# Performance work log

Hardware: AMD Instinct MI355X
Metric: run time of the kernel (lower is better)

## Reference

```python
import jax, jax.numpy as jnp
import numpy as np

EMBED = 1024
HEADS = 16
HEAD_DIM = EMBED // HEADS


def setup_inputs() -> dict:
    key = jax.random.key(0)
    ks = jax.random.split(key, 12)
    B, S = 2, 2048
    inp = {
        "query": jax.random.normal(ks[0], (B, S, EMBED), dtype=jnp.float32),
        "key": jax.random.normal(ks[1], (B, S, EMBED), dtype=jnp.float32),
        "value": jax.random.normal(ks[2], (B, S, EMBED), dtype=jnp.float32),
        "mask": jnp.ones((B, 1, 1, S), dtype=jnp.int32),
    }
    scale = 1.0 / np.sqrt(EMBED)
    inp["Wq"] = jax.random.normal(ks[3], (EMBED, EMBED), dtype=jnp.float32) * scale
    inp["bq"] = jax.random.normal(ks[4], (EMBED,), dtype=jnp.float32) * 0.01
    inp["Wk"] = jax.random.normal(ks[5], (EMBED, EMBED), dtype=jnp.float32) * scale
    inp["bk"] = jax.random.normal(ks[6], (EMBED,), dtype=jnp.float32) * 0.01
    inp["Wv"] = jax.random.normal(ks[7], (EMBED, EMBED), dtype=jnp.float32) * scale
    inp["bv"] = jax.random.normal(ks[8], (EMBED,), dtype=jnp.float32) * 0.01
    inp["Wo"] = jax.random.normal(ks[9], (EMBED, EMBED), dtype=jnp.float32) * scale
    inp["bo"] = jax.random.normal(ks[10], (EMBED,), dtype=jnp.float32) * 0.01
    return inp


def reference(query, key, value, mask, Wq, bq, Wk, bk, Wv, bv, Wo, bo):
    N, Lq, _ = query.shape
    Lk = key.shape[1]
    # Linear projections (torch Linear: x @ W.T + b)
    q = (query @ Wq.T + bq).reshape(N, Lq, HEADS, HEAD_DIM)
    k = (key @ Wk.T + bk).reshape(N, Lk, HEADS, HEAD_DIM)
    v = (value @ Wv.T + bv).reshape(N, Lk, HEADS, HEAD_DIM)
    # scores: [N, H, Lq, Lk]
    energy = jnp.einsum("nqhd,nkhd->nhqk", q, k)
    energy = jnp.where(mask == 0, jnp.float32(-1e20), energy)
    # NOTE: original scales by sqrt(embedSize), not sqrt(head_dim)
    attn = jax.nn.softmax(energy / jnp.sqrt(jnp.float32(EMBED)), axis=3)
    out = jnp.einsum("nhqv,nvhd->nqhd", attn, v).reshape(N, Lq, EMBED)
    return out @ Wo.T + bo
```

## Files before the change

### kernel.cpp

```cpp
#include <hip/hip_runtime.h>
#include <stdint.h>

typedef unsigned short u16;
typedef __attribute__((ext_vector_type(8))) short short8;
typedef __attribute__((ext_vector_type(4))) short short4v;
typedef __attribute__((ext_vector_type(4))) float floatx4;

#define AS_GLOBAL __attribute__((address_space(1)))
#define AS_LDS    __attribute__((address_space(3)))

#define QSCALE 0.045084220f

__device__ __forceinline__ float bf2f(u16 u) {
  union { unsigned int i; float f; } x; x.i = ((unsigned int)u) << 16; return x.f;
}
__device__ __forceinline__ u16 f2bf(float f) {
  union { float f; unsigned int i; } x; x.f = f;
  unsigned int u = x.i;
  u += 0x7fffu + ((u >> 16) & 1u);
  return (u16)(u >> 16);
}
__device__ __forceinline__ u16 f2bf_fast(float f) {
  union { float f; unsigned int i; } x; x.f = f;
  return (u16)((x.i + 0x8000u) >> 16);
}

__device__ __forceinline__ int probe_is_f32(const void* p) {
  const unsigned int* w = (const unsigned int*)p;
  int cnt = 0;
#pragma unroll
  for (int i = 0; i < 64; ++i) {
    unsigned int lo = w[i] & 0xFFFFu;
    int e = (int)((lo >> 7) & 0xFFu);
    cnt += (e >= 117 && e <= 137) ? 1 : 0;
  }
  return cnt < 32;
}

__device__ __forceinline__ short8 ld8(const void* P, size_t off, int isf32) {
  if (isf32) {
    const float* q = (const float*)P + off;
    float4 x = *(const float4*)q;
    float4 y = *(const float4*)(q + 4);
    short8 r;
    r[0] = (short)f2bf(x.x); r[1] = (short)f2bf(x.y);
    r[2] = (short)f2bf(x.z); r[3] = (short)f2bf(x.w);
    r[4] = (short)f2bf(y.x); r[5] = (short)f2bf(y.y);
    r[6] = (short)f2bf(y.z); r[7] = (short)f2bf(y.w);
    return r;
  }
  return *(const short8*)((const u16*)P + off);
}

__device__ __forceinline__ float ldscalar(const void* P, size_t idx, int isf32) {
  return isf32 ? ((const float*)P)[idx] : bf2f(((const u16*)P)[idx]);
}

__global__ __launch_bounds__(256) void cvt7(
    const void* s0, const void* s1, const void* s2, const void* s3,
    const void* s4, const void* s5, const void* s6,
    u16* d0, u16* d1, u16* d2, u16* d3, u16* d4, u16* d5, u16* d6)
{
  const int z = blockIdx.y;
  const void* src; u16* dst; int n;
  switch (z) {
    case 0: src = s0; dst = d0; n = 4194304; break;
    case 1: src = s1; dst = d1; n = 4194304; break;
    case 2: src = s2; dst = d2; n = 4194304; break;
    case 3: src = s3; dst = d3; n = 1048576; break;
    case 4: src = s4; dst = d4; n = 1048576; break;
    case 5: src = s5; dst = d5; n = 1048576; break;
    default: src = s6; dst = d6; n = 1048576; break;
  }
  const int isf32 = probe_is_f32(src);
  for (int i = blockIdx.x * 256 + threadIdx.x; i * 4 < n; i += gridDim.x * 256) {
    if (isf32) {
      float4 x = ((const float4*)src)[i];
      short4v r;
      r[0] = (short)f2bf(x.x); r[1] = (short)f2bf(x.y);
      r[2] = (short)f2bf(x.z); r[3] = (short)f2bf(x.w);
      *(short4v*)(dst + (size_t)i * 4) = r;
    } else {
      *(short4v*)(dst + (size_t)i * 4) = ((const short4v*)src)[i];
    }
  }
}

__device__ __forceinline__ void gemm_core_bf16(
    const u16* __restrict__ A, const u16* __restrict__ W,
    u16* As, u16* Bs, floatx4 acc[4][4], int m0, int n0, int K, int tid)
{
  const int lane = tid & 63, wv = tid >> 6;
  const int wm = wv >> 1, wn = wv & 1;
  const int g = lane >> 4, ml = lane & 15;

  for (int kt = 0; kt < K; kt += 64) {
#pragma unroll
    for (int t = 0; t < 4; ++t) {
      int s = tid + t * 256;
      int row = s >> 3, chp = s & 7;
      int ch = chp ^ (row & 7);
      __builtin_amdgcn_global_load_lds(
          (const AS_GLOBAL unsigned int*)(A + (size_t)(m0 + row) * K + kt + ch * 8),
          (AS_LDS unsigned int*)(As + (size_t)((tid & 448) + t * 256) * 8), 16, 0, 0);
      __builtin_amdgcn_global_load_lds(
          (const AS_GLOBAL unsigned int*)(W + (size_t)(n0 + row) * K + kt + ch * 8),
          (AS_LDS unsigned int*)(Bs + (size_t)((tid & 448) + t * 256) * 8), 16, 0, 0);
    }
    __syncthreads();
#pragma unroll
    for (int kk = 0; kk < 2; ++kk) {
      short8 af[4], bf[4];
#pragma unroll
      for (int i = 0; i < 4; ++i) {
        int row = wm * 64 + i * 16 + ml;
        af[i] = *(const short8*)(As + row * 64 + (((kk << 2) + g) ^ (ml & 7)) * 8);
      }
#pragma unroll
      for (int j = 0; j < 4; ++j) {
        int row = wn * 64 + j * 16 + ml;
        bf[j] = *(const short8*)(Bs + row * 64 + (((kk << 2) + g) ^ (ml & 7)) * 8);
      }
#pragma unroll
      for (int i = 0; i < 4; ++i)
#pragma unroll
        for (int j = 0; j < 4; ++j)
          acc[i][j] = __builtin_amdgcn_mfma_f32_16x16x32_bf16(af[i], bf[j], acc[i][j], 0, 0, 0);
    }
    __syncthreads();
  }
}

__device__ __forceinline__ void gemm_core_cvt(
    const void* __restrict__ A, const void* __restrict__ W, int aF32, int bF32,
    u16* As, u16* Bs, floatx4 acc[4][4], int m0, int n0, int K, int tid)
{
  const int lane = tid & 63, wv = tid >> 6;
  const int wm = wv >> 1, wn = wv & 1;
  const int g = lane >> 4, ml = lane & 15;
  const int r0 = tid >> 2, kc = (tid & 3) << 3;
  const size_t offA0 = (size_t)(m0 + r0) * K + kc;
  const size_t offA1 = (size_t)(m0 + r0 + 64) * K + kc;
  const size_t offB0 = (size_t)(n0 + r0) * K + kc;
  const size_t offB1 = (size_t)(n0 + r0 + 64) * K + kc;
  u16* Al0 = As + tid * 8;  u16* Al1 = As + (tid + 256) * 8;
  u16* Bl0 = Bs + tid * 8;  u16* Bl1 = Bs + (tid + 256) * 8;
  for (int kt = 0; kt < K; kt += 32) {
    short8 a0 = ld8(A, offA0 + kt, aF32);
    short8 a1 = ld8(A, offA1 + kt, aF32);
    short8 b0 = ld8(W, offB0 + kt, bF32);
    short8 b1 = ld8(W, offB1 + kt, bF32);
    *(short8*)Al0 = a0;  *(short8*)Al1 = a1;
    *(short8*)Bl0 = b0;  *(short8*)Bl1 = b1;
    __syncthreads();
    short8 af[4], bf[4];
#pragma unroll
    for (int i = 0; i < 4; ++i)
      af[i] = *(const short8*)(As + (wm * 64 + i * 16 + ml) * 32 + g * 8);
#pragma unroll
    for (int j = 0; j < 4; ++j)
      bf[j] = *(const short8*)(Bs + (wn * 64 + j * 16 + ml) * 32 + g * 8);
#pragma unroll
    for (int i = 0; i < 4; ++i)
#pragma unroll
      for (int j = 0; j < 4; ++j)
        acc[i][j] = __builtin_amdgcn_mfma_f32_16x16x32_bf16(af[i], bf[j], acc[i][j], 0, 0, 0);
    __syncthreads();
  }
}

__device__ __forceinline__ void qkv_epilogue(
    floatx4 acc[4][4], const void* Bi, int cF32, u16* O, int m0, int n0,
    int tid, int z)
{
  const int lane = tid & 63, wv = tid >> 6;
  const int wm = wv >> 1, wn = wv & 1, g = lane >> 4, ml = lane & 15;
  const float sc = (z == 0) ? QSCALE : 1.0f;
#pragma unroll
  for (int j = 0; j < 4; ++j) {
    int gn = n0 + wn * 64 + j * 16 + ml;
    float bvv = ldscalar(Bi, (size_t)gn, cF32);
    int h = gn >> 6, d = gn & 63;
    if (z == 2) {
#pragma unroll
      for (int i = 0; i < 4; ++i) {
        int gm0 = m0 + wm * 64 + i * 16 + g * 4;
        int b = gm0 >> 11, s0 = gm0 & 2047;
        short4v pk;
#pragma unroll
        for (int r = 0; r < 4; ++r) pk[r] = (short)f2bf_fast(acc[i][j][r] + bvv);
        *(short4v*)(O + ((((size_t)b * 16 + h) * 64 + d) * 2048 + s0)) = pk;
      }
    } else {
#pragma unroll
      for (int i = 0; i < 4; ++i)
#pragma unroll
        for (int r = 0; r < 4; ++r) {
          int gm = m0 + wm * 64 + i * 16 + g * 4 + r;
          int b = gm >> 11, s = gm & 2047;
          O[(((size_t)b * 16 + h) * 2048 + s) * 64 + d] =
              f2bf_fast((acc[i][j][r] + bvv) * sc);
        }
    }
  }
}

__global__ __launch_bounds__(256) void qkv_gemm_bf16(
    const u16* __restrict__ Xq, const u16* __restrict__ Xk, const u16* __restrict__ Xv,
    const u16* __restrict__ Wq, const u16* __restrict__ Wk, const u16* __restrict__ Wv,
    const void* __restrict__ Bq, const void* __restrict__ Bk, const void* __restrict__ Bv,
    u16* __restrict__ Oq, u16* __restrict__ Ok, u16* __restrict__ Ov)
{
  __align__(16) __shared__ u16 As[8192];
  __align__(16) __shared__ u16 Bs[8192];
  const int z = blockIdx.z;
  const u16* X = (z == 0) ? Xq : (z == 1) ? Xk : Xv;
  const u16* W = (z == 0) ? Wq : (z == 1) ? Wk : Wv;
  const void* Bi = (z == 0) ? Bq : (z == 1) ? Bk : Bv;
  u16* O = (z == 0) ? Oq : (z == 1) ? Ok : Ov;
  const int cF32 = probe_is_f32(Bi);
  const int tid = threadIdx.x;
  const int m0 = blockIdx.y * 128, n0 = blockIdx.x * 128;
  floatx4 acc[4][4] = {};
  gemm_core_bf16(X, W, As, Bs, acc, m0, n0, 1024, tid);
  qkv_epilogue(acc, Bi, cF32, O, m0, n0, tid, z);
}

__global__ __launch_bounds__(256) void qkv_gemm_cvt(
    const void* __restrict__ Xq, const void* __restrict__ Xk, const void* __restrict__ Xv,
    const void* __restrict__ Wq, const void* __restrict__ Wk, const void* __restrict__ Wv,
    const void* __restrict__ Bq, const void* __restrict__ Bk, const void* __restrict__ Bv,
    u16* __restrict__ Oq, u16* __restrict__ Ok, u16* __restrict__ Ov)
{
  __align__(16) __shared__ u16 As[4096];
  __align__(16) __shared__ u16 Bs[4096];
  const int z = blockIdx.z;
  const void* X  = (z == 0) ? Xq : (z == 1) ? Xk : Xv;
  const void* W  = (z == 0) ? Wq : (z == 1) ? Wk : Wv;
  const void* Bi = (z == 0) ? Bq : (z == 1) ? Bk : Bv;
  u16* O = (z == 0) ? Oq : (z == 1) ? Ok : Ov;
  const int aF32 = probe_is_f32(X);
  const int bF32 = probe_is_f32(W);
  const int cF32 = probe_is_f32(Bi);
  const int tid = threadIdx.x;
  const int m0 = blockIdx.y * 128, n0 = blockIdx.x * 128;
  floatx4 acc[4][4] = {};
  gemm_core_cvt(X, W, aF32, bF32, As, Bs, acc, m0, n0, 1024, tid);
  qkv_epilogue(acc, Bi, cF32, O, m0, n0, tid, z);
}

__device__ __forceinline__ void out_epilogue(
    floatx4 acc[4][4], const void* Bi, int cF32, float* O, int m0, int n0, int tid)
{
  const int lane = tid & 63, wv = tid >> 6;
  const int wm = wv >> 1, wn = wv & 1, g = lane >> 4, ml = lane & 15;
#pragma unroll
  for (int j = 0; j < 4; ++j) {
    int gn = n0 + wn * 64 + j * 16 + ml;
    float bvv = ldscalar(Bi, (size_t)gn, cF32);
#pragma unroll
    for (int i = 0; i < 4; ++i)
#pragma unroll
      for (int r = 0; r < 4; ++r) {
        int gm = m0 + wm * 64 + i * 16 + g * 4 + r;
        O[(size_t)gm * 1024 + gn] = acc[i][j][r] + bvv;
      }
  }
}

__global__ __launch_bounds__(256) void out_gemm_bf16(
    const u16* __restrict__ X, const u16* __restrict__ W,
    const void* __restrict__ Bi, float* __restrict__ O)
{
  __align__(16) __shared__ u16 As[8192];
  __align__(16) __shared__ u16 Bs[8192];
  const int cF32 = probe_is_f32(Bi);
  const int tid = threadIdx.x;
  const int m0 = blockIdx.y * 128, n0 = blockIdx.x * 128;
  floatx4 acc[4][4] = {};
  gemm_core_bf16(X, W, As, Bs, acc, m0, n0, 1024, tid);
  out_epilogue(acc, Bi, cF32, O, m0, n0, tid);
}

__global__ __launch_bounds__(256) void out_gemm_cvt(
    const u16* __restrict__ X, const void* __restrict__ W,
    const void* __restrict__ Bi, float* __restrict__ O)
{
  __align__(16) __shared__ u16 As[4096];
  __align__(16) __shared__ u16 Bs[4096];
  const int bF32 = probe_is_f32(W);
  const int cF32 = probe_is_f32(Bi);
  const int tid = threadIdx.x;
  const int m0 = blockIdx.y * 128, n0 = blockIdx.x * 128;
  floatx4 acc[4][4] = {};
  gemm_core_cvt(X, W, 0, bF32, As, Bs, acc, m0, n0, 1024, tid);
  out_epilogue(acc, Bi, cF32, O, m0, n0, tid);
}

__global__ __launch_bounds__(256) void flash_attn(
    const u16* __restrict__ Q, const u16* __restrict__ K, const u16* __restrict__ V,
    const int* __restrict__ Mask, u16* __restrict__ O)
{
  __align__(16) __shared__ u16 Ks[128 * 64];
  __align__(16) __shared__ u16 Vt[64 * 128];
  __align__(16) __shared__ u16 Ps[4][16 * 136];
  __align__(16) __shared__ int Ms[128];
  __shared__ int Wok[4];

  const int qt = blockIdx.x;
  const int bh = blockIdx.y;
  const int b = bh >> 4, h = bh & 15;
  const int tid = threadIdx.x;
  const int lane = tid & 63, wv = tid >> 6;
  const int g = lane >> 4, ml = lane & 15;

  const size_t baseQ  = (((size_t)b * 16 + h) * 2048 + (size_t)qt * 64) * 64;
  const size_t baseKV = ((size_t)b * 16 + h) * 2048 * 64;

  {
    int la = 1;
#pragma unroll
    for (int i = 0; i < 8; ++i) la &= Mask[b * 2048 + tid * 8 + i];
    int wall = __all(la != 0);
    if (lane == 0) Wok[wv] = wall;
  }

  short8 qf[2];
#pragma unroll
  for (int ks = 0; ks < 2; ++ks)
    qf[ks] = *(const short8*)(Q + baseQ + (size_t)(wv * 16 + ml) * 64 + ks * 32 + g * 8);

  const u16* kg[4]; const u16* vg[4];
  u16* kl[4]; u16* vl[4];
#pragma unroll
  for (int t = 0; t < 4; ++t) {
    int s = tid + t * 256;
    int krow = s >> 3, kch = (s & 7) ^ (krow & 7);
    kg[t] = K + baseKV + (size_t)krow * 64 + kch * 8;
    int vd = s >> 4, vch = (s & 15) ^ (vd & 15);
    vg[t] = V + baseKV + (size_t)vd * 2048 + vch * 8;
    kl[t] = Ks + (size_t)((tid & 448) + t * 256) * 8;
    vl[t] = Vt + (size_t)((tid & 448) + t * 256) * 8;
  }

  __syncthreads();
  const bool maskall = Wok[0] && Wok[1] && Wok[2] && Wok[3];

  floatx4 oacc[4] = {};
  float lp[4] = {0.f, 0.f, 0.f, 0.f};

  for (int kv0 = 0; kv0 < 2048; kv0 += 128) {
    __syncthreads();
#pragma unroll
    for (int t = 0; t < 4; ++t) {
      __builtin_amdgcn_global_load_lds((const AS_GLOBAL unsigned int*)kg[t],
                                       (AS_LDS unsigned int*)kl[t], 16, 0, 0);
      __builtin_amdgcn_global_load_lds((const AS_GLOBAL unsigned int*)vg[t],
                                       (AS_LDS unsigned int*)vl[t], 16, 0, 0);
      kg[t] += 128 * 64;
      vg[t] += 128;
    }
    if (!maskall && tid < 128) Ms[tid] = Mask[b * 2048 + kv0 + tid];
    __syncthreads();

    float sv[8][4];
#pragma unroll
    for (int j = 0; j < 8; ++j) {
      floatx4 a = {0.f, 0.f, 0.f, 0.f};
      int row = j * 16 + ml;
#pragma unroll
      for (int ks = 0; ks < 2; ++ks) {
        short8 kb = *(const short8*)(Ks + row * 64 + ((((ks << 2) + g) ^ (ml & 7)) << 3));
        a = __builtin_amdgcn_mfma_f32_16x16x32_bf16(qf[ks], kb, a, 0, 0, 0);
      }
#pragma unroll
      for (int r = 0; r < 4; ++r) sv[j][r] = a[r];
    }
    if (!maskall) {
      int mok[8];
#pragma unroll
      for (int j = 0; j < 8; ++j) mok[j] = Ms[j * 16 + ml];
#pragma unroll
      for (int j = 0; j < 8; ++j)
#pragma unroll
        for (int r = 0; r < 4; ++r)
          sv[j][r] = (mok[j] == 0) ? -1.0e30f : sv[j][r];
    }

#pragma unroll
    for (int j = 0; j < 8; ++j)
#pragma unroll
      for (int r = 0; r < 4; ++r) {
        float p = __builtin_amdgcn_exp2f(fminf(sv[j][r], 80.f));
        sv[j][r] = p;
        lp[r] += p;
      }

#pragma unroll
    for (int j = 0; j < 8; ++j)
#pragma unroll
      for (int r = 0; r < 4; ++r)
        Ps[wv][(g * 4 + r) * 136 + j * 16 + ml] = f2bf_fast(sv[j][r]);

    __asm__ __volatile__("s_waitcnt lgkmcnt(0)" ::: "memory");

    short8 pa[4];
#pragma unroll
    for (int j2 = 0; j2 < 4; ++j2)
      pa[j2] = *(const short8*)(&Ps[wv][ml * 136 + j2 * 32 + g * 8]);
#pragma unroll
    for (int t = 0; t < 4; ++t)
#pragma unroll
      for (int j2 = 0; j2 < 4; ++j2) {
        short8 vb = *(const short8*)(Vt + (t * 16 + ml) * 128 + ((((j2 << 2) + g) ^ ml) << 3));
        oacc[t] = __builtin_amdgcn_mfma_f32_16x16x32_bf16(pa[j2], vb, oacc[t], 0, 0, 0);
      }
  }

  float inv[4];
#pragma unroll
  for (int r = 0; r < 4; ++r) {
    float l = lp[r];
    l += __shfl_xor(l, 1);
    l += __shfl_xor(l, 2);
    l += __shfl_xor(l, 4);
    l += __shfl_xor(l, 8);
    inv[r] = (l > 0.f) ? 1.0f / l : 0.f;
  }
#pragma unroll
  for (int t = 0; t < 4; ++t)
#pragma unroll
    for (int r = 0; r < 4; ++r) {
      int q = qt * 64 + wv * 16 + g * 4 + r;
      int d = t * 16 + ml;
      O[((size_t)b * 2048 + q) * 1024 + h * 64 + d] = f2bf_fast(oacc[t][r] * inv[r]);
    }
}

extern "C" void kernel_launch(void* const* d_in, const int* in_sizes, int n_in,
                              void* d_out, int out_size, void* d_ws, size_t ws_size,
                              hipStream_t stream) {
  const void* q_in = d_in[0];
  const void* k_in = d_in[1];
  const void* v_in = d_in[2];
  const int* mask = (const int*)d_in[3];
  const void* Wq = d_in[4];  const void* bq = d_in[5];
  const void* Wk = d_in[6];  const void* bk = d_in[7];
  const void* Wv = d_in[8];  const void* bv = d_in[9];
  const void* Wo = d_in[10]; const void* bo = d_in[11];

  const size_t NTOK = (size_t)2 * 2048 * 1024;
  const size_t NW   = (size_t)1024 * 1024;

  if (ws_size >= (size_t)67108864) {
    u16* CXq = (u16*)d_ws;
    u16* CXk = CXq + NTOK;
    u16* CXv = CXk + NTOK;
    u16* CWq = CXv + NTOK;
    u16* CWk = CWq + NW;
    u16* CWv = CWk + NW;
    u16* CWo = CWv + NW;
    u16* Qp  = CWo + NW;
    u16* Kp  = Qp + NTOK;
    u16* Vp  = Kp + NTOK;
    u16* Ao  = Vp + NTOK;

    cvt7<<<dim3(1024, 7), 256, 0, stream>>>(q_in, k_in, v_in, Wq, Wk, Wv, Wo,
                                            CXq, CXk, CXv, CWq, CWk, CWv, CWo);
    qkv_gemm_bf16<<<dim3(8, 32, 3), 256, 0, stream>>>(CXq, CXk, CXv,
                                                      CWq, CWk, CWv,
                                                      bq, bk, bv, Qp, Kp, Vp);
    flash_attn<<<dim3(32, 32), 256, 0, stream>>>(Qp, Kp, Vp, mask, Ao);
    out_gemm_bf16<<<dim3(8, 32), 256, 0, stream>>>(Ao, CWo, bo, (float*)d_out);
  } else {
    u16* Qp = (u16*)d_ws;
    u16* Kp = Qp + NTOK;
    u16* Vp = Kp + NTOK;
    u16* Ao = Vp + NTOK;

    qkv_gemm_cvt<<<dim3(8, 32, 3), 256, 0, stream>>>(q_in, k_in, v_in,
                                                     Wq, Wk, Wv, bq, bk, bv,
                                                     Qp, Kp, Vp);
    flash_attn<<<dim3(32, 32), 256, 0, stream>>>(Qp, Kp, Vp, mask, Ao);
    out_gemm_cvt<<<dim3(8, 32), 256, 0, stream>>>(Ao, Wo, bo, (float*)d_out);
  }
}
```

Baseline: 263.8 us.

## Shrink GEMM K-tiles and flash KV tiles; narrow output GEMM N-tile

The bf16 GEMM core now loads K-tiles of 32 instead of 64, without the XOR swizzle, which halves LDS use per block. The output projection GEMM becomes its own kernel with a 128x64 tile and twice as many blocks, to fill more CUs. Flash attention switches from 128 to 64 KV rows per iteration, with smaller LDS buffers and the swizzle indices adjusted to match. It also drops the exp2 input clamp. The aim is higher occupancy and better CU coverage, at the cost of more barriers per unit of work, possible LDS bank conflicts from the unswizzled GEMM layout, and less MFMA work between syncs.

```diff
diff --git a/kernel.cpp b/kernel.cpp
--- a/kernel.cpp
+++ b/kernel.cpp
@@ -93,40 +93,36 @@
   const int lane = tid & 63, wv = tid >> 6;
   const int wm = wv >> 1, wn = wv & 1;
   const int g = lane >> 4, ml = lane & 15;
-
-  for (int kt = 0; kt < K; kt += 64) {
-#pragma unroll
-    for (int t = 0; t < 4; ++t) {
-      int s = tid + t * 256;
-      int row = s >> 3, chp = s & 7;
-      int ch = chp ^ (row & 7);
-      __builtin_amdgcn_global_load_lds(
-          (const AS_GLOBAL unsigned int*)(A + (size_t)(m0 + row) * K + kt + ch * 8),
-          (AS_LDS unsigned int*)(As + (size_t)((tid & 448) + t * 256) * 8), 16, 0, 0);
-      __builtin_amdgcn_global_load_lds(
-          (const AS_GLOBAL unsigned int*)(W + (size_t)(n0 + row) * K + kt + ch * 8),
-          (AS_LDS unsigned int*)(Bs + (size_t)((tid & 448) + t * 256) * 8), 16, 0, 0);
-    }
-    __syncthreads();
-#pragma unroll
-    for (int kk = 0; kk < 2; ++kk) {
-      short8 af[4], bf[4];
-#pragma unroll
-      for (int i = 0; i < 4; ++i) {
-        int row = wm * 64 + i * 16 + ml;
-        af[i] = *(const short8*)(As + row * 64 + (((kk << 2) + g) ^ (ml & 7)) * 8);
-      }
-#pragma unroll
-      for (int j = 0; j < 4; ++j) {
-        int row = wn * 64 + j * 16 + ml;
-        bf[j] = *(const short8*)(Bs + row * 64 + (((kk << 2) + g) ^ (ml & 7)) * 8);
-      }
-#pragma unroll
-      for (int i = 0; i < 4; ++i)
-#pragma unroll
-        for (int j = 0; j < 4; ++j)
-          acc[i][j] = __builtin_amdgcn_mfma_f32_16x16x32_bf16(af[i], bf[j], acc[i][j], 0, 0, 0);
-    }
+  const int r0 = tid >> 2, kc = (tid & 3) << 3;
+  const u16* Ag0 = A + (size_t)(m0 + r0) * K + kc;
+  const u16* Ag1 = A + (size_t)(m0 + r0 + 64) * K + kc;
+  const u16* Bg0 = W + (size_t)(n0 + r0) * K + kc;
+  const u16* Bg1 = W + (size_t)(n0 + r0 + 64) * K + kc;
+  u16* Al0 = As + tid * 8;  u16* Al1 = As + (tid + 256) * 8;
+  u16* Bl0 = Bs + tid * 8;  u16* Bl1 = Bs + (tid + 256) * 8;
+
+  for (int kt = 0; kt < K; kt += 32) {
+    __builtin_amdgcn_global_load_lds((const AS_GLOBAL unsigned int*)(Ag0 + kt),
+                                     (AS_LDS unsigned int*)Al0, 16, 0, 0);
+    __builtin_amdgcn_global_load_lds((const AS_GLOBAL unsigned int*)(Ag1 + kt),
+                                     (AS_LDS unsigned int*)Al1, 16, 0, 0);
+    __builtin_amdgcn_global_load_lds((const AS_GLOBAL unsigned int*)(Bg0 + kt),
+                                     (AS_LDS unsigned int*)Bl0, 16, 0, 0);
+    __builtin_amdgcn_global_load_lds((const AS_GLOBAL unsigned int*)(Bg1 + kt),
+                                     (AS_LDS unsigned int*)Bl1, 16, 0, 0);
+    __syncthreads();
+    short8 af[4], bf[4];
+#pragma unroll
+    for (int i = 0; i < 4; ++i)
+      af[i] = *(const short8*)(As + (wm * 64 + i * 16 + ml) * 32 + g * 8);
+#pragma unroll
+    for (int j = 0; j < 4; ++j)
+      bf[j] = *(const short8*)(Bs + (wn * 64 + j * 16 + ml) * 32 + g * 8);
+#pragma unroll
+    for (int i = 0; i < 4; ++i)
+#pragma unroll
+      for (int j = 0; j < 4; ++j)
+        acc[i][j] = __builtin_amdgcn_mfma_f32_16x16x32_bf16(af[i], bf[j], acc[i][j], 0, 0, 0);
     __syncthreads();
   }
 }
@@ -211,8 +207,8 @@
     const void* __restrict__ Bq, const void* __restrict__ Bk, const void* __restrict__ Bv,
     u16* __restrict__ Oq, u16* __restrict__ Ok, u16* __restrict__ Ov)
 {
-  __align__(16) __shared__ u16 As[8192];
-  __align__(16) __shared__ u16 Bs[8192];
+  __align__(16) __shared__ u16 As[4096];
+  __align__(16) __shared__ u16 Bs[4096];
   const int z = blockIdx.z;
   const u16* X = (z == 0) ? Xq : (z == 1) ? Xk : Xv;
   const u16* W = (z == 0) ? Wq : (z == 1) ? Wk : Wv;
@@ -249,14 +245,51 @@
   qkv_epilogue(acc, Bi, cF32, O, m0, n0, tid, z);
 }
 
-__device__ __forceinline__ void out_epilogue(
-    floatx4 acc[4][4], const void* Bi, int cF32, float* O, int m0, int n0, int tid)
-{
+__global__ __launch_bounds__(256) void out_gemm_bf16(
+    const u16* __restrict__ X, const u16* __restrict__ W,
+    const void* __restrict__ Bi, float* __restrict__ O)
+{
+  __align__(16) __shared__ u16 As[4096];
+  __align__(16) __shared__ u16 Bs[2048];
+  const int cF32 = probe_is_f32(Bi);
+  const int tid = threadIdx.x;
   const int lane = tid & 63, wv = tid >> 6;
-  const int wm = wv >> 1, wn = wv & 1, g = lane >> 4, ml = lane & 15;
-#pragma unroll
-  for (int j = 0; j < 4; ++j) {
-    int gn = n0 + wn * 64 + j * 16 + ml;
+  const int wm = wv >> 1, wn = wv & 1;
+  const int g = lane >> 4, ml = lane & 15;
+  const int m0 = blockIdx.y * 128, n0 = blockIdx.x * 64;
+  const int r0 = tid >> 2, kc = (tid & 3) << 3;
+  const u16* Ag0 = X + (size_t)(m0 + r0) * 1024 + kc;
+  const u16* Ag1 = X + (size_t)(m0 + r0 + 64) * 1024 + kc;
+  const u16* Bg0 = W + (size_t)(n0 + r0) * 1024 + kc;
+  u16* Al0 = As + tid * 8;  u16* Al1 = As + (tid + 256) * 8;
+  u16* Bl0 = Bs + tid * 8;
+
+  floatx4 acc[4][2] = {};
+  for (int kt = 0; kt < 1024; kt += 32) {
+    __builtin_amdgcn_global_load_lds((const AS_GLOBAL unsigned int*)(Ag0 + kt),
+                                     (AS_LDS unsigned int*)Al0, 16, 0, 0);
+    __builtin_amdgcn_global_load_lds((const AS_GLOBAL unsigned int*)(Ag1 + kt),
+                                     (AS_LDS unsigned int*)Al1, 16, 0, 0);
+    __builtin_amdgcn_global_load_lds((const AS_GLOBAL unsigned int*)(Bg0 + kt),
+                                     (AS_LDS unsigned int*)Bl0, 16, 0, 0);
+    __syncthreads();
+    short8 af[4], bf[2];
+#pragma unroll
+    for (int i = 0; i < 4; ++i)
+      af[i] = *(const short8*)(As + (wm * 64 + i * 16 + ml) * 32 + g * 8);
+#pragma unroll
+    for (int j = 0; j < 2; ++j)
+      bf[j] = *(const short8*)(Bs + (wn * 32 + j * 16 + ml) * 32 + g * 8);
+#pragma unroll
+    for (int i = 0; i < 4; ++i)
+#pragma unroll
+      for (int j = 0; j < 2; ++j)
+        acc[i][j] = __builtin_amdgcn_mfma_f32_16x16x32_bf16(af[i], bf[j], acc[i][j], 0, 0, 0);
+    __syncthreads();
+  }
+#pragma unroll
+  for (int j = 0; j < 2; ++j) {
+    int gn = n0 + wn * 32 + j * 16 + ml;
     float bvv = ldscalar(Bi, (size_t)gn, cF32);
 #pragma unroll
     for (int i = 0; i < 4; ++i)
@@ -266,20 +299,6 @@
         O[(size_t)gm * 1024 + gn] = acc[i][j][r] + bvv;
       }
   }
-}
-
-__global__ __launch_bounds__(256) void out_gemm_bf16(
-    const u16* __restrict__ X, const u16* __restrict__ W,
-    const void* __restrict__ Bi, float* __restrict__ O)
-{
-  __align__(16) __shared__ u16 As[8192];
-  __align__(16) __shared__ u16 Bs[8192];
-  const int cF32 = probe_is_f32(Bi);
-  const int tid = threadIdx.x;
-  const int m0 = blockIdx.y * 128, n0 = blockIdx.x * 128;
-  floatx4 acc[4][4] = {};
-  gemm_core_bf16(X, W, As, Bs, acc, m0, n0, 1024, tid);
-  out_epilogue(acc, Bi, cF32, O, m0, n0, tid);
 }
 
 __global__ __launch_bounds__(256) void out_gemm_cvt(
@@ -294,17 +313,30 @@
   const int m0 = blockIdx.y * 128, n0 = blockIdx.x * 128;
   floatx4 acc[4][4] = {};
   gemm_core_cvt(X, W, 0, bF32, As, Bs, acc, m0, n0, 1024, tid);
-  out_epilogue(acc, Bi, cF32, O, m0, n0, tid);
+  const int lane = tid & 63, wv = tid >> 6;
+  const int wm = wv >> 1, wn = wv & 1, g = lane >> 4, ml = lane & 15;
+#pragma unroll
+  for (int j = 0; j < 4; ++j) {
+    int gn = n0 + wn * 64 + j * 16 + ml;
+    float bvv = ldscalar(Bi, (size_t)gn, cF32);
+#pragma unroll
+    for (int i = 0; i < 4; ++i)
+#pragma unroll
+      for (int r = 0; r < 4; ++r) {
+        int gm = m0 + wm * 64 + i * 16 + g * 4 + r;
+        O[(size_t)gm * 1024 + gn] = acc[i][j][r] + bvv;
+      }
+  }
 }
 
 __global__ __launch_bounds__(256) void flash_attn(
     const u16* __restrict__ Q, const u16* __restrict__ K, const u16* __restrict__ V,
     const int* __restrict__ Mask, u16* __restrict__ O)
 {
-  __align__(16) __shared__ u16 Ks[128 * 64];
-  __align__(16) __shared__ u16 Vt[64 * 128];
-  __align__(16) __shared__ u16 Ps[4][16 * 136];
-  __align__(16) __shared__ int Ms[128];
+  __align__(16) __shared__ u16 Ks[64 * 64];
+  __align__(16) __shared__ u16 Vt[64 * 64];
+  __align__(16) __shared__ u16 Ps[4][16 * 72];
+  __align__(16) __shared__ int Ms[64];
   __shared__ int Wok[4];
 
   const int qt = blockIdx.x;
@@ -330,14 +362,14 @@
   for (int ks = 0; ks < 2; ++ks)
     qf[ks] = *(const short8*)(Q + baseQ + (size_t)(wv * 16 + ml) * 64 + ks * 32 + g * 8);
 
-  const u16* kg[4]; const u16* vg[4];
-  u16* kl[4]; u16* vl[4];
-#pragma unroll
-  for (int t = 0; t < 4; ++t) {
+  const u16* kg[2]; const u16* vg[2];
+  u16* kl[2]; u16* vl[2];
+#pragma unroll
+  for (int t = 0; t < 2; ++t) {
     int s = tid + t * 256;
     int krow = s >> 3, kch = (s & 7) ^ (krow & 7);
     kg[t] = K + baseKV + (size_t)krow * 64 + kch * 8;
-    int vd = s >> 4, vch = (s & 15) ^ (vd & 15);
+    int vd = s >> 3,  vch = (s & 7) ^ (vd & 7);
     vg[t] = V + baseKV + (size_t)vd * 2048 + vch * 8;
     kl[t] = Ks + (size_t)((tid & 448) + t * 256) * 8;
     vl[t] = Vt + (size_t)((tid & 448) + t * 256) * 8;
@@ -349,70 +381,70 @@
   floatx4 oacc[4] = {};
   float lp[4] = {0.f, 0.f, 0.f, 0.f};
 
-  for (int kv0 = 0; kv0 < 2048; kv0 += 128) {
-    __syncthreads();
-#pragma unroll
-    for (int t = 0; t < 4; ++t) {
+  for (int kv0 = 0; kv0 < 2048; kv0 += 64) {
+    __syncthreads();
+#pragma unroll
+    for (int t = 0; t < 2; ++t) {
       __builtin_amdgcn_global_load_lds((const AS_GLOBAL unsigned int*)kg[t],
                                        (AS_LDS unsigned int*)kl[t], 16, 0, 0);
       __builtin_amdgcn_global_load_lds((const AS_GLOBAL unsigned int*)vg[t],
                                        (AS_LDS unsigned int*)vl[t], 16, 0, 0);
-      kg[t] += 128 * 64;
-      vg[t] += 128;
+      kg[t] += 64 * 64;
+      vg[t] += 64;
     }
-    if (!maskall && tid < 128) Ms[tid] = Mask[b * 2048 + kv0 + tid];
-    __syncthreads();
-
-    float sv[8][4];
-#pragma unroll
-    for (int j = 0; j < 8; ++j) {
+    if (!maskall && tid < 64) Ms[tid] = Mask[b * 2048 + kv0 + tid];
+    __syncthreads();
+
+    float sv[4][4];
+#pragma unroll
+    for (int j = 0; j < 4; ++j) {
       floatx4 a = {0.f, 0.f, 0.f, 0.f};
       int row = j * 16 + ml;
 #pragma unroll
       for (int ks = 0; ks < 2; ++ks) {
-        short8 kb = *(const short8*)(Ks + row * 64 + ((((ks << 2) + g) ^ (ml & 7)) << 3));
+        short8 kb = *(const short8*)(Ks + row * 64 + ((((ks << 2) + g) ^ (row & 7)) << 3));
         a = __builtin_amdgcn_mfma_f32_16x16x32_bf16(qf[ks], kb, a, 0, 0, 0);
       }
 #pragma unroll
       for (int r = 0; r < 4; ++r) sv[j][r] = a[r];
     }
     if (!maskall) {
-      int mok[8];
-#pragma unroll
-      for (int j = 0; j < 8; ++j) mok[j] = Ms[j * 16 + ml];
-#pragma unroll
-      for (int j = 0; j < 8; ++j)
+      int mok[4];
+#pragma unroll
+      for (int j = 0; j < 4; ++j) mok[j] = Ms[j * 16 + ml];
+#pragma unroll
+      for (int j = 0; j < 4; ++j)
 #pragma unroll
         for (int r = 0; r < 4; ++r)
           sv[j][r] = (mok[j] == 0) ? -1.0e30f : sv[j][r];
     }
 
 #pragma unroll
-    for (int j = 0; j < 8; ++j)
+    for (int j = 0; j < 4; ++j)
 #pragma unroll
       for (int r = 0; r < 4; ++r) {
-        float p = __builtin_amdgcn_exp2f(fminf(sv[j][r], 80.f));
+        float p = __builtin_amdgcn_exp2f(sv[j][r]);
         sv[j][r] = p;
         lp[r] += p;
       }
 
 #pragma unroll
-    for (int j = 0; j < 8; ++j)
+    for (int j = 0; j < 4; ++j)
 #pragma unroll
       for (int r = 0; r < 4; ++r)
-        Ps[wv][(g * 4 + r) * 136 + j * 16 + ml] = f2bf_fast(sv[j][r]);
+        Ps[wv][(g * 4 + r) * 72 + j * 16 + ml] = f2bf_fast(sv[j][r]);
 
     __asm__ __volatile__("s_waitcnt lgkmcnt(0)" ::: "memory");
 
-    short8 pa[4];
-#pragma unroll
-    for (int j2 = 0; j2 < 4; ++j2)
-      pa[j2] = *(const short8*)(&Ps[wv][ml * 136 + j2 * 32 + g * 8]);
+    short8 pa[2];
+#pragma unroll
+    for (int j2 = 0; j2 < 2; ++j2)
+      pa[j2] = *(const short8*)(&Ps[wv][ml * 72 + j2 * 32 + g * 8]);
 #pragma unroll
     for (int t = 0; t < 4; ++t)
 #pragma unroll
-      for (int j2 = 0; j2 < 4; ++j2) {
-        short8 vb = *(const short8*)(Vt + (t * 16 + ml) * 128 + ((((j2 << 2) + g) ^ ml) << 3));
+      for (int j2 = 0; j2 < 2; ++j2) {
+        short8 vb = *(const short8*)(Vt + (t * 16 + ml) * 64 + ((((j2 << 2) + g) ^ (ml & 7)) << 3));
         oacc[t] = __builtin_amdgcn_mfma_f32_16x16x32_bf16(pa[j2], vb, oacc[t], 0, 0, 0);
       }
   }
@@ -471,7 +503,7 @@
                                                       CWq, CWk, CWv,
                                                       bq, bk, bv, Qp, Kp, Vp);
     flash_attn<<<dim3(32, 32), 256, 0, stream>>>(Qp, Kp, Vp, mask, Ao);
-    out_gemm_bf16<<<dim3(8, 32), 256, 0, stream>>>(Ao, CWo, bo, (float*)d_out);
+    out_gemm_bf16<<<dim3(16, 32), 256, 0, stream>>>(Ao, CWo, bo, (float*)d_out);
   } else {
     u16* Qp = (u16*)d_ws;
     u16* Kp = Qp + NTOK;
```

New measurement: 260.2 us. About the same (-1.4%).
